# Kernel tuning notes

Hardware: AMD Instinct MI355X
Metric: run time of the kernel (lower is better)

The kernel has to match this reference:

```python
import jax, jax.numpy as jnp
import numpy as np

N = 50000
E = 800000
IN_DIM = 128
OUT_DIM = 128
HEADS = 4
HEAD_DIM = OUT_DIM // HEADS  # 32


def setup_inputs() -> dict:
    key = jax.random.key(0)
    k1, k2, k3, k4 = jax.random.split(key, 4)
    x = jax.random.normal(k1, (N, IN_DIM), dtype=jnp.float32)
    edge_index = jax.random.randint(k2, (2, E), 0, N, dtype=jnp.int32)
    # nn.Linear(in_dim, out_dim): weight [out_dim, in_dim]
    W = jax.random.normal(k3, (OUT_DIM, IN_DIM), dtype=jnp.float32) * (1.0 / np.sqrt(IN_DIM))
    # nn.Linear(2*head_dim, 1): weight [1, 2*head_dim] -> flattened [2*head_dim]
    a_w = jax.random.normal(k4, (2 * HEAD_DIM,), dtype=jnp.float32) * (1.0 / np.sqrt(2 * HEAD_DIM))
    return {"x": x, "edge_index": edge_index, "W": W, "a_w": a_w}


def reference(x, edge_index, W, a_w):
    n = x.shape[0]
    Wx = (x @ W.T).reshape(n, HEADS, HEAD_DIM)          # [N,H,D]
    src, dst = edge_index[0], edge_index[1]
    Wx_src = Wx[src]                                     # [E,H,D]
    Wx_dst = Wx[dst]                                     # [E,H,D]
    # a([Wx_src || Wx_dst]) = Wx_src @ a_src + Wx_dst @ a_dst
    a_src, a_dst = a_w[:HEAD_DIM], a_w[HEAD_DIM:]
    e = jnp.einsum('ehd,d->eh', Wx_src, a_src) + jnp.einsum('ehd,d->eh', Wx_dst, a_dst)
    e = jax.nn.leaky_relu(e, negative_slope=0.2)         # [E,H]
    # numerically-stable segment softmax over incoming edges of each dst node
    e_max = jax.ops.segment_max(e, dst, num_segments=n)  # [N,H], -inf for empty
    e_exp = jnp.exp(e - e_max[dst])                      # [E,H]
    denom = jax.ops.segment_sum(e_exp, dst, num_segments=n)  # [N,H]
    alpha = e_exp / (denom[dst] + 1e-8)                  # [E,H] (dropout=0 -> identity)
    weighted = alpha[..., None] * Wx_src                 # [E,H,D]
    out = jax.ops.segment_sum(weighted, dst, num_segments=n)  # [N,H,D]
    return jax.nn.elu(out.reshape(n, OUT_DIM))
```

## Files before the change

### kernel.cpp

```cpp
#include <hip/hip_runtime.h>
#include <hip/hip_bf16.h>
#include <math.h>

#define HEADS 4
#define NBKT 196
#define CAPB 4608
#define CAPQ 1792

typedef short bf16x8 __attribute__((ext_vector_type(8)));
typedef float f32x4 __attribute__((ext_vector_type(4)));
typedef unsigned short ushort8 __attribute__((ext_vector_type(8)));

__device__ __forceinline__ float lrelu(float v) { return v >= 0.f ? v : 0.2f * v; }

__device__ __forceinline__ unsigned short f2bf(float f) {
    unsigned u = __float_as_uint(f);
    return (unsigned short)((u + 0x7FFF + ((u >> 16) & 1)) >> 16);
}

__device__ __forceinline__ unsigned pk2bf(float a, float b) {
    __hip_bfloat162 h = __float22bfloat162_rn(make_float2(a, b));
    unsigned u;
    __builtin_memcpy(&u, &h, 4);
    return u;
}

__global__ __launch_bounds__(256, 2) void fused_kernel(const float* __restrict__ x,
                                                       const float* __restrict__ W,
                                                       const float* __restrict__ aw,
                                                       const int* __restrict__ ei,
                                                       unsigned short* __restrict__ Wxh,
                                                       float* __restrict__ s_src,
                                                       float* __restrict__ s_dst,
                                                       int* __restrict__ gcur,
                                                       unsigned* __restrict__ gbuf,
                                                       int n, int E, int ngemm) {
    __shared__ __align__(16) char smem[66304];
    const int t = threadIdx.x;

    if ((int)blockIdx.x < ngemm) {
        unsigned short* Alds = (unsigned short*)smem;
        unsigned short* Blds = (unsigned short*)(smem + 32768);
        float* sawm = (float*)(smem + 65536);
        const int w = t >> 6, l = t & 63;
        const int q = l >> 4, l16 = l & 15;
        const int node0 = blockIdx.x * 128;

        if (t < 64) sawm[t] = aw[t];
        if (blockIdx.x == 0) {
            if (t < 4) s_src[(size_t)n * 4 + t] = -1e30f;
            if (t < 64) ((unsigned*)(Wxh + (size_t)n * 128))[t] = 0u;
        }

#pragma unroll
        for (int i = 0; i < 8; ++i) {
            int c = i * 256 + t;
            int nl = c >> 4, k8 = c & 15;
            int gn = node0 + nl;
            if (gn >= n) gn = n - 1;
            const float4* gp = (const float4*)(x + (size_t)gn * 128 + k8 * 8);
            float4 v0 = gp[0], v1 = gp[1];
            uint4 u = make_uint4(pk2bf(v0.x, v0.y), pk2bf(v0.z, v0.w),
                                 pk2bf(v1.x, v1.y), pk2bf(v1.z, v1.w));
            int ch = (((nl >> 4) * 4 + (k8 >> 2)) * 4 + (k8 & 3)) * 16 + (nl & 15);
            *(uint4*)(&Alds[ch * 8]) = u;
        }
#pragma unroll
        for (int i = 0; i < 8; ++i) {
            int c = i * 256 + t;
            int dl = c >> 4, k8 = c & 15;
            const float4* gp = (const float4*)(W + (size_t)dl * 128 + k8 * 8);
            float4 v0 = gp[0], v1 = gp[1];
            uint4 u = make_uint4(pk2bf(v0.x, v0.y), pk2bf(v0.z, v0.w),
                                 pk2bf(v1.x, v1.y), pk2bf(v1.z, v1.w));
            int ch = (((dl >> 4) * 4 + (k8 >> 2)) * 4 + (k8 & 3)) * 16 + (dl & 15);
            *(uint4*)(&Blds[ch * 8]) = u;
        }
        __syncthreads();

        f32x4 acc[2][8];
#pragma unroll
        for (int rt = 0; rt < 2; ++rt)
#pragma unroll
            for (int ct = 0; ct < 8; ++ct) acc[rt][ct] = (f32x4){0.f, 0.f, 0.f, 0.f};

#pragma unroll
        for (int kk = 0; kk < 4; ++kk) {
            bf16x8 a0 = *(const bf16x8*)(&Alds[(((w * 2 + 0) * 4 + kk) * 64 + l) * 8]);
            bf16x8 a1 = *(const bf16x8*)(&Alds[(((w * 2 + 1) * 4 + kk) * 64 + l) * 8]);
#pragma unroll
            for (int ct = 0; ct < 8; ++ct) {
                bf16x8 b = *(const bf16x8*)(&Blds[((ct * 4 + kk) * 64 + l) * 8]);
                acc[0][ct] = __builtin_amdgcn_mfma_f32_16x16x32_bf16(a0, b, acc[0][ct], 0, 0, 0);
                acc[1][ct] = __builtin_amdgcn_mfma_f32_16x16x32_bf16(a1, b, acc[1][ct], 0, 0, 0);
            }
        }

        __syncthreads();
#pragma unroll
        for (int rt = 0; rt < 2; ++rt) {
            int nl = w * 32 + rt * 16 + q * 4;
#pragma unroll
            for (int ct = 0; ct < 8; ++ct) {
                int dim = ct * 16 + l16;
                Alds[(nl + 0) * 128 + dim] = f2bf(acc[rt][ct][0]);
                Alds[(nl + 1) * 128 + dim] = f2bf(acc[rt][ct][1]);
                Alds[(nl + 2) * 128 + dim] = f2bf(acc[rt][ct][2]);
                Alds[(nl + 3) * 128 + dim] = f2bf(acc[rt][ct][3]);
            }
        }
        __syncthreads();

#pragma unroll
        for (int i = 0; i < 8; ++i) {
            int c = i * 256 + t;
            int nl = c >> 4, d8 = c & 15;
            int gn = node0 + nl;
            ushort8 u = *(const ushort8*)(&Alds[nl * 128 + d8 * 8]);
            if (gn < n) *(ushort8*)(Wxh + (size_t)gn * 128 + d8 * 8) = u;
            float sp = 0.f, dp = 0.f;
            int ab = (d8 & 3) * 8;
#pragma unroll
            for (int j = 0; j < 8; ++j) {
                float v = __uint_as_float(((unsigned)(unsigned short)u[j]) << 16);
                sp += v * sawm[ab + j];
                dp += v * sawm[32 + ab + j];
            }
            sp += __shfl_xor(sp, 1, 64); dp += __shfl_xor(dp, 1, 64);
            sp += __shfl_xor(sp, 2, 64); dp += __shfl_xor(dp, 2, 64);
            if ((l & 3) == 0 && gn < n) {
                int h = (l & 15) >> 2;
                s_src[(size_t)gn * 4 + h] = sp;
                s_dst[(size_t)gn * 4 + h] = dp;
            }
        }
    } else {
        int* hist = (int*)smem;
        int* scanws = (int*)(smem + 1024);
        int* lbase = (int*)(smem + 2048);
        int* lcur = (int*)(smem + 3072);
        int* gb = (int*)(smem + 4096);
        unsigned* sorted = (unsigned*)(smem + 5120);
        unsigned char* bkt = (unsigned char*)(smem + 21504);

        const int blk = blockIdx.x - ngemm;
        const int b0 = blk * 4096;
        const int total = min(4096, E - b0);

        hist[t] = 0;
        __syncthreads();

        unsigned pk[16];
#pragma unroll
        for (int i = 0; i < 16; ++i) {
            int idx = i * 256 + t;
            if (idx < total) {
                int e = b0 + idx;
                unsigned s = (unsigned)ei[e], d = (unsigned)ei[E + e];
                pk[i] = s | (d << 16);
                atomicAdd(&hist[d >> 8], 1);
            }
        }
        __syncthreads();
        int v = hist[t];
        scanws[t] = v;
        __syncthreads();
        for (int off = 1; off < 256; off <<= 1) {
            int y = (t >= off) ? scanws[t - off] : 0;
            __syncthreads();
            scanws[t] += y;
            __syncthreads();
        }
        int ex = scanws[t] - v;
        lbase[t] = ex;
        lcur[t] = ex;
        if (t < NBKT) gb[t] = (v > 0) ? atomicAdd(&gcur[t], v) : 0;
        __syncthreads();
#pragma unroll
        for (int i = 0; i < 16; ++i) {
            int idx = i * 256 + t;
            if (idx < total) {
                int b = pk[i] >> 24;
                int qpos = atomicAdd(&lcur[b], 1);
                sorted[qpos] = pk[i];
                bkt[qpos] = (unsigned char)b;
            }
        }
        __syncthreads();
#pragma unroll
        for (int i = 0; i < 16; ++i) {
            int s = i * 256 + t;
            if (s < total) {
                int b = bkt[s];
                int pos = gb[b] + (s - lbase[b]);
                if (pos < CAPB) gbuf[(size_t)b * CAPB + pos] = sorted[s];
            }
        }
    }
}

__global__ __launch_bounds__(256) void pass2_accum(const int* __restrict__ gcur,
                                                   const unsigned* __restrict__ gbuf,
                                                   const float* __restrict__ s_src,
                                                   const float* __restrict__ s_dst,
                                                   const unsigned short* __restrict__ Wxh,
                                                   float* __restrict__ out, int n) {
    __shared__ int hist[64], basew[64], cur[64];
    __shared__ __align__(16) unsigned short csrl[CAPQ];
    const int t = threadIdx.x;
    const int bucket = blockIdx.x >> 2;
    const unsigned quarter = blockIdx.x & 3;
    int cnt = gcur[bucket];
    if (cnt > CAPB) cnt = CAPB;
    const unsigned* gp = gbuf + (size_t)bucket * CAPB;

    if (t < 64) hist[t] = 0;
    __syncthreads();

    unsigned pk[18];
#pragma unroll
    for (int i = 0; i < 18; ++i) {
        int idx = i * 256 + t;
        pk[i] = 0xFFFFFFFFu;
        if (idx < cnt) {
            unsigned u = gp[idx];
            if (((u >> 22) & 3u) == quarter) {
                pk[i] = u;
                atomicAdd(&hist[(u >> 16) & 63], 1);
            }
        }
    }
    __syncthreads();

    if (t < 64) {
        int v = hist[t];
        int vp = (v + 7) & ~7;
        int sc = vp;
#pragma unroll
        for (int off = 1; off < 64; off <<= 1) {
            int y = __shfl_up(sc, off, 64);
            if (t >= off) sc += y;
        }
        int base = sc - vp;
        basew[t] = base;
        cur[t] = base;
        for (int j = v; j < vp; ++j) {
            int pos = base + j;
            if (pos < CAPQ) csrl[pos] = (unsigned short)n;
        }
        hist[t] = vp;
    }
    __syncthreads();

#pragma unroll
    for (int i = 0; i < 18; ++i) {
        unsigned u = pk[i];
        if (u != 0xFFFFFFFFu) {
            int bin = (u >> 16) & 63;
            int pos = atomicAdd(&cur[bin], 1);
            if (pos < CAPQ) csrl[pos] = (unsigned short)(u & 0xFFFF);
        }
    }
    __syncthreads();

    const int wid = t >> 6, lane = t & 63;
    const int l = lane & 15, grp = lane >> 4, h = l >> 2;
    const unsigned ONE2 = 0x3F803F80u;

    for (int ln = wid; ln < 64; ln += 4) {
        int node = bucket * 256 + (int)quarter * 64 + ln;
        if (node >= n) break;
        int start = basew[ln];
        int npairs = hist[ln] >> 1;
        float sdn = s_dst[(size_t)node * 4 + h];

        float acc[8] = {0.f, 0.f, 0.f, 0.f, 0.f, 0.f, 0.f, 0.f};
        float dsum = 0.f;
        int p = grp;
        for (; p + 4 < npairs; p += 8) {
            unsigned c0 = *(const unsigned*)(&csrl[start + 2 * p]);
            unsigned c1 = *(const unsigned*)(&csrl[start + 2 * (p + 4)]);
            int sa0 = c0 & 0xFFFF, sa1 = c0 >> 16;
            int sb0 = c1 & 0xFFFF, sb1 = c1 >> 16;
            uint4 Ua0 = *(const uint4*)(Wxh + ((size_t)sa0 << 7) + l * 8);
            uint4 Ua1 = *(const uint4*)(Wxh + ((size_t)sa1 << 7) + l * 8);
            uint4 Ub0 = *(const uint4*)(Wxh + ((size_t)sb0 << 7) + l * 8);
            uint4 Ub1 = *(const uint4*)(Wxh + ((size_t)sb1 << 7) + l * 8);
            float wa0 = __expf(lrelu(s_src[sa0 * 4 + h] + sdn));
            float wa1 = __expf(lrelu(s_src[sa1 * 4 + h] + sdn));
            float wb0 = __expf(lrelu(s_src[sb0 * 4 + h] + sdn));
            float wb1 = __expf(lrelu(s_src[sb1 * 4 + h] + sdn));
            unsigned wpa = pk2bf(wa0, wa1);
            unsigned wpb = pk2bf(wb0, wb1);
            asm("v_dot2_f32_bf16 %0, %1, %2, %0" : "+v"(dsum) : "v"(wpa), "v"(ONE2));
            asm("v_dot2_f32_bf16 %0, %1, %2, %0" : "+v"(dsum) : "v"(wpb), "v"(ONE2));
            unsigned a0[4] = {Ua0.x, Ua0.y, Ua0.z, Ua0.w};
            unsigned a1[4] = {Ua1.x, Ua1.y, Ua1.z, Ua1.w};
            unsigned b0[4] = {Ub0.x, Ub0.y, Ub0.z, Ub0.w};
            unsigned b1[4] = {Ub1.x, Ub1.y, Ub1.z, Ub1.w};
#pragma unroll
            for (int j = 0; j < 4; ++j) {
                unsigned lo_a = __builtin_amdgcn_perm(a0[j], a1[j], 0x01000504u);
                unsigned hi_a = __builtin_amdgcn_perm(a0[j], a1[j], 0x03020706u);
                unsigned lo_b = __builtin_amdgcn_perm(b0[j], b1[j], 0x01000504u);
                unsigned hi_b = __builtin_amdgcn_perm(b0[j], b1[j], 0x03020706u);
                asm("v_dot2_f32_bf16 %0, %1, %2, %0" : "+v"(acc[2 * j]) : "v"(wpa), "v"(lo_a));
                asm("v_dot2_f32_bf16 %0, %1, %2, %0" : "+v"(acc[2 * j + 1]) : "v"(wpa), "v"(hi_a));
                asm("v_dot2_f32_bf16 %0, %1, %2, %0" : "+v"(acc[2 * j]) : "v"(wpb), "v"(lo_b));
                asm("v_dot2_f32_bf16 %0, %1, %2, %0" : "+v"(acc[2 * j + 1]) : "v"(wpb), "v"(hi_b));
            }
        }
        if (p < npairs) {
            unsigned c0 = *(const unsigned*)(&csrl[start + 2 * p]);
            int sa0 = c0 & 0xFFFF, sa1 = c0 >> 16;
            uint4 Ua0 = *(const uint4*)(Wxh + ((size_t)sa0 << 7) + l * 8);
            uint4 Ua1 = *(const uint4*)(Wxh + ((size_t)sa1 << 7) + l * 8);
            float wa0 = __expf(lrelu(s_src[sa0 * 4 + h] + sdn));
            float wa1 = __expf(lrelu(s_src[sa1 * 4 + h] + sdn));
            unsigned wpa = pk2bf(wa0, wa1);
            asm("v_dot2_f32_bf16 %0, %1, %2, %0" : "+v"(dsum) : "v"(wpa), "v"(ONE2));
            unsigned a0[4] = {Ua0.x, Ua0.y, Ua0.z, Ua0.w};
            unsigned a1[4] = {Ua1.x, Ua1.y, Ua1.z, Ua1.w};
#pragma unroll
            for (int j = 0; j < 4; ++j) {
                unsigned lo_a = __builtin_amdgcn_perm(a0[j], a1[j], 0x01000504u);
                unsigned hi_a = __builtin_amdgcn_perm(a0[j], a1[j], 0x03020706u);
                asm("v_dot2_f32_bf16 %0, %1, %2, %0" : "+v"(acc[2 * j]) : "v"(wpa), "v"(lo_a));
                asm("v_dot2_f32_bf16 %0, %1, %2, %0" : "+v"(acc[2 * j + 1]) : "v"(wpa), "v"(hi_a));
            }
        }
#pragma unroll
        for (int m = 16; m <= 32; m <<= 1) {
#pragma unroll
            for (int j = 0; j < 8; ++j) acc[j] += __shfl_xor(acc[j], m, 64);
            dsum += __shfl_xor(dsum, m, 64);
        }
        if (grp == 0) {
            float inv = 1.f / (dsum + 1e-8f);
            float o[8];
#pragma unroll
            for (int j = 0; j < 8; ++j) {
                float v = acc[j] * inv;
                o[j] = v > 0.f ? v : (__expf(v) - 1.f);
            }
            float4* dp = (float4*)(out + (size_t)node * 128 + l * 8);
            dp[0] = make_float4(o[0], o[1], o[2], o[3]);
            dp[1] = make_float4(o[4], o[5], o[6], o[7]);
        }
    }
}

extern "C" void kernel_launch(void* const* d_in, const int* in_sizes, int n_in,
                              void* d_out, int out_size, void* d_ws, size_t ws_size,
                              hipStream_t stream) {
    const float* x = (const float*)d_in[0];
    const int* ei = (const int*)d_in[1];
    const float* W = (const float*)d_in[2];
    const float* aw = (const float*)d_in[3];
    float* out = (float*)d_out;
    const int n = in_sizes[0] / 128;
    const int E = in_sizes[1] / 2;

    char* ws = (char*)d_ws;
    size_t off = 0;
    unsigned short* Wxh = (unsigned short*)(ws + off); off += (size_t)(n + 8) * 128 * 2;
    float* s_src = (float*)(ws + off);     off += (size_t)(n + 1) * HEADS * 4;
    float* s_dst = (float*)(ws + off);     off += (size_t)n * HEADS * 4;
    int* gcur = (int*)(ws + off);          off += 1024;
    unsigned* gbuf = (unsigned*)(ws + off); off += (size_t)NBKT * CAPB * 4;

    const int ngemm = (n + 127) / 128;
    const int npass1 = (E + 4095) / 4096;

    hipMemsetAsync(gcur, 0, 1024, stream);
    fused_kernel<<<ngemm + npass1, 256, 0, stream>>>(x, W, aw, ei, Wxh, s_src, s_dst,
                                                     gcur, gbuf, n, E, ngemm);
    pass2_accum<<<NBKT * 4, 256, 0, stream>>>(gcur, gbuf, s_src, s_dst, Wxh, out, n);
}
```

Baseline: 140.9 us.

## Load GEMM A operand directly from global to halve LDS and double pass2 block size

The GEMM part of the fused kernel no longer stages x into LDS. Each lane loads its MFMA A fragment straight from global memory, converts it to bf16 in registers, and reuses the B buffer for the output transpose. This halves the static LDS footprint, which allows three blocks per CU instead of two. The pass2 accumulation kernel moves to 512 threads per block, so each thread keeps half as many packed edges and eight waves share the node loop. The trade-offs are less coalesced x loads and higher register pressure under the tighter launch bounds.

```diff
diff --git a/kernel.cpp b/kernel.cpp
--- a/kernel.cpp
+++ b/kernel.cpp
@@ -25,7 +25,7 @@
     return u;
 }
 
-__global__ __launch_bounds__(256, 2) void fused_kernel(const float* __restrict__ x,
+__global__ __launch_bounds__(256, 3) void fused_kernel(const float* __restrict__ x,
                                                        const float* __restrict__ W,
                                                        const float* __restrict__ aw,
                                                        const int* __restrict__ ei,
@@ -35,13 +35,12 @@
                                                        int* __restrict__ gcur,
                                                        unsigned* __restrict__ gbuf,
                                                        int n, int E, int ngemm) {
-    __shared__ __align__(16) char smem[66304];
+    __shared__ __align__(16) char smem[33280];
     const int t = threadIdx.x;
 
     if ((int)blockIdx.x < ngemm) {
-        unsigned short* Alds = (unsigned short*)smem;
-        unsigned short* Blds = (unsigned short*)(smem + 32768);
-        float* sawm = (float*)(smem + 65536);
+        unsigned short* Blds = (unsigned short*)smem;
+        float* sawm = (float*)(smem + 32768);
         const int w = t >> 6, l = t & 63;
         const int q = l >> 4, l16 = l & 15;
         const int node0 = blockIdx.x * 128;
@@ -52,19 +51,6 @@
             if (t < 64) ((unsigned*)(Wxh + (size_t)n * 128))[t] = 0u;
         }
 
-#pragma unroll
-        for (int i = 0; i < 8; ++i) {
-            int c = i * 256 + t;
-            int nl = c >> 4, k8 = c & 15;
-            int gn = node0 + nl;
-            if (gn >= n) gn = n - 1;
-            const float4* gp = (const float4*)(x + (size_t)gn * 128 + k8 * 8);
-            float4 v0 = gp[0], v1 = gp[1];
-            uint4 u = make_uint4(pk2bf(v0.x, v0.y), pk2bf(v0.z, v0.w),
-                                 pk2bf(v1.x, v1.y), pk2bf(v1.z, v1.w));
-            int ch = (((nl >> 4) * 4 + (k8 >> 2)) * 4 + (k8 & 3)) * 16 + (nl & 15);
-            *(uint4*)(&Alds[ch * 8]) = u;
-        }
 #pragma unroll
         for (int i = 0; i < 8; ++i) {
             int c = i * 256 + t;
@@ -84,10 +70,26 @@
 #pragma unroll
             for (int ct = 0; ct < 8; ++ct) acc[rt][ct] = (f32x4){0.f, 0.f, 0.f, 0.f};
 
+        int g0 = node0 + w * 32 + l16;
+        int g1 = g0 + 16;
+        if (g0 >= n) g0 = n - 1;
+        if (g1 >= n) g1 = n - 1;
+        const float* xr0 = x + (size_t)g0 * 128 + q * 8;
+        const float* xr1 = x + (size_t)g1 * 128 + q * 8;
+
 #pragma unroll
         for (int kk = 0; kk < 4; ++kk) {
-            bf16x8 a0 = *(const bf16x8*)(&Alds[(((w * 2 + 0) * 4 + kk) * 64 + l) * 8]);
-            bf16x8 a1 = *(const bf16x8*)(&Alds[(((w * 2 + 1) * 4 + kk) * 64 + l) * 8]);
+            const float4* pa0 = (const float4*)(xr0 + kk * 32);
+            const float4* pa1 = (const float4*)(xr1 + kk * 32);
+            float4 v0 = pa0[0], v1 = pa0[1];
+            float4 v2 = pa1[0], v3 = pa1[1];
+            uint4 ua0 = make_uint4(pk2bf(v0.x, v0.y), pk2bf(v0.z, v0.w),
+                                   pk2bf(v1.x, v1.y), pk2bf(v1.z, v1.w));
+            uint4 ua1 = make_uint4(pk2bf(v2.x, v2.y), pk2bf(v2.z, v2.w),
+                                   pk2bf(v3.x, v3.y), pk2bf(v3.z, v3.w));
+            bf16x8 a0, a1;
+            __builtin_memcpy(&a0, &ua0, 16);
+            __builtin_memcpy(&a1, &ua1, 16);
 #pragma unroll
             for (int ct = 0; ct < 8; ++ct) {
                 bf16x8 b = *(const bf16x8*)(&Blds[((ct * 4 + kk) * 64 + l) * 8]);
@@ -103,10 +105,10 @@
 #pragma unroll
             for (int ct = 0; ct < 8; ++ct) {
                 int dim = ct * 16 + l16;
-                Alds[(nl + 0) * 128 + dim] = f2bf(acc[rt][ct][0]);
-                Alds[(nl + 1) * 128 + dim] = f2bf(acc[rt][ct][1]);
-                Alds[(nl + 2) * 128 + dim] = f2bf(acc[rt][ct][2]);
-                Alds[(nl + 3) * 128 + dim] = f2bf(acc[rt][ct][3]);
+                Blds[(nl + 0) * 128 + dim] = f2bf(acc[rt][ct][0]);
+                Blds[(nl + 1) * 128 + dim] = f2bf(acc[rt][ct][1]);
+                Blds[(nl + 2) * 128 + dim] = f2bf(acc[rt][ct][2]);
+                Blds[(nl + 3) * 128 + dim] = f2bf(acc[rt][ct][3]);
             }
         }
         __syncthreads();
@@ -116,7 +118,7 @@
             int c = i * 256 + t;
             int nl = c >> 4, d8 = c & 15;
             int gn = node0 + nl;
-            ushort8 u = *(const ushort8*)(&Alds[nl * 128 + d8 * 8]);
+            ushort8 u = *(const ushort8*)(&Blds[nl * 128 + d8 * 8]);
             if (gn < n) *(ushort8*)(Wxh + (size_t)gn * 128 + d8 * 8) = u;
             float sp = 0.f, dp = 0.f;
             int ab = (d8 & 3) * 8;
@@ -199,7 +201,7 @@
     }
 }
 
-__global__ __launch_bounds__(256) void pass2_accum(const int* __restrict__ gcur,
+__global__ __launch_bounds__(512) void pass2_accum(const int* __restrict__ gcur,
                                                    const unsigned* __restrict__ gbuf,
                                                    const float* __restrict__ s_src,
                                                    const float* __restrict__ s_dst,
@@ -217,10 +219,10 @@
     if (t < 64) hist[t] = 0;
     __syncthreads();
 
-    unsigned pk[18];
-#pragma unroll
-    for (int i = 0; i < 18; ++i) {
-        int idx = i * 256 + t;
+    unsigned pk[9];
+#pragma unroll
+    for (int i = 0; i < 9; ++i) {
+        int idx = i * 512 + t;
         pk[i] = 0xFFFFFFFFu;
         if (idx < cnt) {
             unsigned u = gp[idx];
@@ -253,7 +255,7 @@
     __syncthreads();
 
 #pragma unroll
-    for (int i = 0; i < 18; ++i) {
+    for (int i = 0; i < 9; ++i) {
         unsigned u = pk[i];
         if (u != 0xFFFFFFFFu) {
             int bin = (u >> 16) & 63;
@@ -267,7 +269,7 @@
     const int l = lane & 15, grp = lane >> 4, h = l >> 2;
     const unsigned ONE2 = 0x3F803F80u;
 
-    for (int ln = wid; ln < 64; ln += 4) {
+    for (int ln = wid; ln < 64; ln += 8) {
         int node = bucket * 256 + (int)quarter * 64 + ln;
         if (node >= n) break;
         int start = basew[ln];
@@ -375,5 +377,5 @@
     hipMemsetAsync(gcur, 0, 1024, stream);
     fused_kernel<<<ngemm + npass1, 256, 0, stream>>>(x, W, aw, ei, Wxh, s_src, s_dst,
                                                      gcur, gbuf, n, E, ngemm);
-    pass2_accum<<<NBKT * 4, 256, 0, stream>>>(gcur, gbuf, s_src, s_dst, Wxh, out, n);
-}
+    pass2_accum<<<NBKT * 4, 512, 0, stream>>>(gcur, gbuf, s_src, s_dst, Wxh, out, n);
+}
```

Result: faster. 134.5 us (-4.5%).
